# Optimization experiments

Measured on AMD Instinct MI355X. Metric: run time of the kernel, lower is better.

## Reference

```python
import jax, jax.numpy as jnp
import numpy as np
from jax import lax

H = 64  # LSTM units (hard-coded in the module)


def _lstm(x, W, U, b, return_sequences):
    """Keras-style LSTM (inference; recurrent_dropout inactive).
    x: [B, T, F]; W: [F, 4H]; U: [H, 4H]; b: [4H].
    Gate order (Keras): i, f, g(cell), o.
    """
    B = x.shape[0]
    # Precompute input contribution for all timesteps: [T, B, 4H]
    xz = jnp.einsum('btf,fg->tbg', x, W) + b

    def step(carry, z_t):
        h, c = carry
        z = z_t + h @ U  # [B, 4H]
        i = jax.nn.sigmoid(z[:, :H])
        f = jax.nn.sigmoid(z[:, H:2 * H])
        g = jnp.tanh(z[:, 2 * H:3 * H])
        o = jax.nn.sigmoid(z[:, 3 * H:])
        c = f * c + i * g
        h = o * jnp.tanh(c)
        return (h, c), h

    init = (jnp.zeros((B, H), x.dtype), jnp.zeros((B, H), x.dtype))
    (h_last, _), hs = lax.scan(step, init, xz)
    if return_sequences:
        return jnp.transpose(hs, (1, 0, 2))  # [B, T, H]
    return h_last  # [B, H]


def setup_inputs() -> dict:
    key = jax.random.key(0)
    ks = jax.random.split(key, 8)
    B, T, F = 4096, 256, 32
    s_in = 1.0 / np.sqrt(F)
    s_h = 1.0 / np.sqrt(H)
    return {
        'x': jax.random.normal(ks[0], (B, T, F), jnp.float32),
        'W1': jax.random.normal(ks[1], (F, 4 * H), jnp.float32) * s_in,
        'U1': jax.random.normal(ks[2], (H, 4 * H), jnp.float32) * s_h,
        'b1': jnp.zeros((4 * H,), jnp.float32),
        'W2': jax.random.normal(ks[3], (H, 4 * H), jnp.float32) * s_h,
        'U2': jax.random.normal(ks[4], (H, 4 * H), jnp.float32) * s_h,
        'b2': jnp.zeros((4 * H,), jnp.float32),
        'Wd': jax.random.normal(ks[5], (H, H), jnp.float32) * s_h,
        'bd': jnp.zeros((H,), jnp.float32),
        'Wo': jax.random.normal(ks[6], (H, 1), jnp.float32) * s_h,
        'bo': jnp.zeros((1,), jnp.float32),
    }


def reference(x, W1, U1, b1, W2, U2, b2, Wd, bd, Wo, bo):
    h_seq = _lstm(x, W1, U1, b1, return_sequences=True)   # hidden_lstm
    h_last = _lstm(h_seq, W2, U2, b2, return_sequences=False)  # lstm_layer
    d = jax.nn.sigmoid(h_last @ Wd + bd)  # Dense(64, sigmoid)
    return jax.nn.sigmoid(d @ Wo + bo)    # Dense(1, sigmoid) -> [B, 1]
```

## Files before the change

kernel.cpp:

```cpp
#include <hip/hip_runtime.h>


typedef __attribute__((ext_vector_type(8))) short short8;
typedef __attribute__((ext_vector_type(4))) float floatx4;
typedef __attribute__((ext_vector_type(2))) float floatx2;

__device__ __forceinline__ float ex2(float x){ return __builtin_amdgcn_exp2f(x); }
__device__ __forceinline__ float rcp_(float x){ return __builtin_amdgcn_rcpf(x); }
__device__ __forceinline__ float sigm(float x){ return rcp_(1.0f + ex2(-1.44269504f*x)); }
__device__ __forceinline__ unsigned bfbits(float f){
    unsigned u = __builtin_bit_cast(unsigned, f);
    u += 0x7FFFu + ((u >> 16) & 1u);
    return u >> 16;
}
__device__ __forceinline__ short f2bf(float f){ return (short)bfbits(f); }
__device__ __forceinline__ unsigned cvtpk(float lo, float hi){
    unsigned r;
    asm("v_cvt_pk_bf16_f32 %0, %1, %2" : "=v"(r) : "v"(lo), "v"(hi));
    return r;
}
__device__ __forceinline__ void wg_barrier_lds(){
    asm volatile("s_waitcnt lgkmcnt(0)\n\ts_barrier" ::: "memory");
}
__device__ __forceinline__ float gate_update(const floatx4& z, float& c){
    float iv = rcp_(1.0f + ex2(z[0]));
    float fv = rcp_(1.0f + ex2(z[1]));
    float rg = rcp_(1.0f + ex2(z[2]));
    float ov = rcp_(1.0f + ex2(z[3]));
    float gp = fmaf(-5.77078016f, rg, 2.88539008f);
    c = fmaf(fv, c, iv * gp);
    float th = fmaf(-2.0f, rcp_(1.0f + ex2(c)), 1.0f);
    return ov * th;
}

#define MFMA_BF16 __builtin_amdgcn_mfma_f32_16x16x32_bf16

__global__ __launch_bounds__(1024, 1)
void lstm2_tz(const float* __restrict__ x,
              const float* __restrict__ W1, const float* __restrict__ U1, const float* __restrict__ b1,
              const float* __restrict__ W2, const float* __restrict__ U2, const float* __restrict__ b2,
              const float* __restrict__ Wd, const float* __restrict__ bd,
              const float* __restrict__ Wo, const float* __restrict__ bo,
              float* __restrict__ out)
{
    __shared__ __align__(16) short h1b[2][16 * 64];
    __shared__ __align__(16) short h2b[2][16 * 64];
    __shared__ __align__(16) short xsb[2][16 * 40];
    __shared__ float psum[4][16];

    const int tid  = threadIdx.x;
    const int w    = tid >> 6;
    const bool isL1 = (w < 8);
    const int wv   = w & 7;
    const int lane = tid & 63;
    const int n    = lane & 15;
    const int q    = lane >> 4;
    const int b0   = blockIdx.x * 16;

    const float LG = 1.44269504f;

    const int ugl = n >> 2;
    const int gA  = n & 3;
    const float sA = (gA == 2) ? (2.0f * LG) : (-LG);

    const int sw   = n & 7;
    const int hro0 = n * 64 + ((q ^ sw) << 3);
    const int hro1 = n * 64 + (((4 + q) ^ sw) << 3);
    const int xro  = n * 40 + q * 8;
    const int hwo  = n * 64 + ((wv ^ sw) << 3) + q * 2;

    short8  Wa[8];
    floatx4 bC[2];
    if (isL1) {
#pragma unroll
        for (int tt = 0; tt < 2; ++tt) {
            const int un   = wv * 8 + ugl * 2 + tt;
            const int ncol = gA * 64 + un;
#pragma unroll
            for (int j = 0; j < 8; ++j) {
                const int k = q * 8 + j;
                Wa[tt * 3 + 0][j] = f2bf(W1[k * 256 + ncol] * sA);
                Wa[tt * 3 + 1][j] = f2bf(U1[k * 256 + ncol] * sA);
                Wa[tt * 3 + 2][j] = f2bf(U1[(32 + k) * 256 + ncol] * sA);
            }
#pragma unroll
            for (int r = 0; r < 4; ++r)
                bC[tt][r] = b1[r * 64 + wv * 8 + q * 2 + tt] * ((r == 2) ? (2.0f * LG) : (-LG));
        }
    } else {
#pragma unroll
        for (int tt = 0; tt < 2; ++tt) {
            const int un   = wv * 8 + ugl * 2 + tt;
            const int ncol = gA * 64 + un;
#pragma unroll
            for (int j = 0; j < 8; ++j) {
                const int k = q * 8 + j;
                Wa[tt * 4 + 0][j] = f2bf(W2[k * 256 + ncol] * sA);
                Wa[tt * 4 + 1][j] = f2bf(W2[(32 + k) * 256 + ncol] * sA);
                Wa[tt * 4 + 2][j] = f2bf(U2[k * 256 + ncol] * sA);
                Wa[tt * 4 + 3][j] = f2bf(U2[(32 + k) * 256 + ncol] * sA);
            }
#pragma unroll
            for (int r = 0; r < 4; ++r)
                bC[tt][r] = b2[r * 64 + wv * 8 + q * 2 + tt] * ((r == 2) ? (2.0f * LG) : (-LG));
        }
    }

    {
        unsigned* p1 = (unsigned*)&h1b[0][0];
        unsigned* p2 = (unsigned*)&h2b[0][0];
        for (int i = tid; i < 1024; i += 1024) { p1[i] = 0u; p2[i] = 0u; }
    }

    const int xr = tid >> 4;
    const int xc = (tid & 15) * 2;
    const float* xrow = x + (size_t)(b0 + xr) * 8192 + xc;
    floatx2 xv0;
    if (tid < 256) {
        floatx2 v = *(const floatx2*)xrow;
        *(unsigned*)&xsb[0][xr * 40 + xc] = cvtpk(v.x, v.y);
        xv0 = *(const floatx2*)(xrow + 32);
    }
    __syncthreads();

    float c[2] = {0, 0};
    floatx4 z[2];

    for (int u = 0; u <= 257; ++u) {
        const int par = u & 1, pax = par ^ 1;

        if (isL1) {
            if (u < 256) {
                const short* hR = &h1b[pax][0];
                short8 bx  = *(const short8*)&xsb[par][xro];
                short8 bh0 = *(const short8*)&hR[hro0];
                short8 bh1 = *(const short8*)&hR[hro1];
                if (tid < 256 && u < 255) {
                    *(unsigned*)&xsb[pax][xr * 40 + xc] = cvtpk(xv0.x, xv0.y);
                    if (u < 254) xv0 = *(const floatx2*)(xrow + (size_t)(u + 2) * 32);
                }
#pragma unroll
                for (int tt = 0; tt < 2; ++tt) {
                    floatx4 zz = bC[tt];
                    zz = MFMA_BF16(Wa[tt * 3 + 0], bx,  zz, 0, 0, 0);
                    zz = MFMA_BF16(Wa[tt * 3 + 1], bh0, zz, 0, 0, 0);
                    zz = MFMA_BF16(Wa[tt * 3 + 2], bh1, zz, 0, 0, 0);
                    z[tt] = zz;
                }
            }
        } else {
            if (u >= 2) {
                float hv0 = gate_update(z[0], c[0]);
                float hv1 = gate_update(z[1], c[1]);
                *(unsigned*)&h2b[par][hwo] = cvtpk(hv0, hv1);
            }
        }
        wg_barrier_lds();

        if (isL1) {
            if (u < 256) {
                float hv0 = gate_update(z[0], c[0]);
                float hv1 = gate_update(z[1], c[1]);
                *(unsigned*)&h1b[par][hwo] = cvtpk(hv0, hv1);
            }
        } else {
            if (u >= 1 && u <= 256) {
                const short* hR = &h1b[pax][0];
                const short* gR = &h2b[par][0];
                short8 bh0 = *(const short8*)&hR[hro0];
                short8 bh1 = *(const short8*)&hR[hro1];
                short8 bg0 = *(const short8*)&gR[hro0];
                short8 bg1 = *(const short8*)&gR[hro1];
#pragma unroll
                for (int tt = 0; tt < 2; ++tt) {
                    floatx4 zz = bC[tt];
                    zz = MFMA_BF16(Wa[tt * 4 + 0], bh0, zz, 0, 0, 0);
                    zz = MFMA_BF16(Wa[tt * 4 + 1], bh1, zz, 0, 0, 0);
                    zz = MFMA_BF16(Wa[tt * 4 + 2], bg0, zz, 0, 0, 0);
                    zz = MFMA_BF16(Wa[tt * 4 + 3], bg1, zz, 0, 0, 0);
                    z[tt] = zz;
                }
            }
        }
        wg_barrier_lds();
    }

    if (!isL1 && wv < 4) {
        const int colD = wv * 16 + n;
        short8 wd0, wd1;
#pragma unroll
        for (int j = 0; j < 8; ++j) {
            wd0[j] = f2bf(Wd[(q * 8 + j) * 64 + colD] * (-LG));
            wd1[j] = f2bf(Wd[(32 + q * 8 + j) * 64 + colD] * (-LG));
        }
        short8 hA0 = *(const short8*)&h2b[1][hro0];
        short8 hA1 = *(const short8*)&h2b[1][hro1];
        const float bdv = bd[colD] * (-LG);
        floatx4 dacc = { bdv, bdv, bdv, bdv };
        dacc = MFMA_BF16(hA0, wd0, dacc, 0, 0, 0);
        dacc = MFMA_BF16(hA1, wd1, dacc, 0, 0, 0);
        const float wo = Wo[colD];
#pragma unroll
        for (int r = 0; r < 4; ++r) {
            float p = rcp_(1.0f + ex2(dacc[r])) * wo;
            p += __shfl_xor(p, 1, 64);
            p += __shfl_xor(p, 2, 64);
            p += __shfl_xor(p, 4, 64);
            p += __shfl_xor(p, 8, 64);
            if (n == 0) psum[wv][q * 4 + r] = p;
        }
    }
    __syncthreads();
    if (tid < 16) {
        float s = psum[0][tid] + psum[1][tid] + psum[2][tid] + psum[3][tid] + bo[0];
        out[b0 + tid] = sigm(s);
    }
}

extern "C" void kernel_launch(void* const* d_in, const int* in_sizes, int n_in,
                              void* d_out, int out_size, void* d_ws, size_t ws_size,
                              hipStream_t stream) {
    (void)in_sizes; (void)n_in; (void)d_ws; (void)ws_size; (void)out_size;
    const float* x  = (const float*)d_in[0];
    const float* W1 = (const float*)d_in[1];
    const float* U1 = (const float*)d_in[2];
    const float* b1 = (const float*)d_in[3];
    const float* W2 = (const float*)d_in[4];
    const float* U2 = (const float*)d_in[5];
    const float* b2 = (const float*)d_in[6];
    const float* Wd = (const float*)d_in[7];
    const float* bd = (const float*)d_in[8];
    const float* Wo = (const float*)d_in[9];
    const float* bo = (const float*)d_in[10];
    lstm2_tz<<<dim3(256), dim3(1024), 0, stream>>>(
        x, W1, U1, b1, W2, U2, b2, Wd, bd, Wo, bo, (float*)d_out);
}
```

Before: 366.7 us.

## Fuse gate update into MFMA phase, halving barriers per step, share reciprocals

Restructures the two-layer wavefront-specialized time loop so each half-step does both the MFMA and the gate nonlinearity, then writes h. This leaves one workgroup barrier per timestep instead of two, and the loop is unrolled by two so buffer parities are compile-time constants. The gate function also replaces four reciprocals with one, computed on the product of the four denominators, with extra multiplies to recover each sigmoid. That shortens the critical path but risks overflow or inf when the product of the exp terms grows large.

```diff
diff --git a/kernel.cpp b/kernel.cpp
--- a/kernel.cpp
+++ b/kernel.cpp
@@ -23,10 +23,17 @@
     asm volatile("s_waitcnt lgkmcnt(0)\n\ts_barrier" ::: "memory");
 }
 __device__ __forceinline__ float gate_update(const floatx4& z, float& c){
-    float iv = rcp_(1.0f + ex2(z[0]));
-    float fv = rcp_(1.0f + ex2(z[1]));
-    float rg = rcp_(1.0f + ex2(z[2]));
-    float ov = rcp_(1.0f + ex2(z[3]));
+    float ea = 1.0f + ex2(z[0]);
+    float eb = 1.0f + ex2(z[1]);
+    float eg = 1.0f + ex2(z[2]);
+    float eo = 1.0f + ex2(z[3]);
+    float ab = ea * eb, gd = eg * eo;
+    float r  = rcp_(ab * gd);
+    float gdr = gd * r, abr = ab * r;
+    float iv = eb * gdr;
+    float fv = ea * gdr;
+    float rg = eo * abr;
+    float ov = eg * abr;
     float gp = fmaf(-5.77078016f, rg, 2.88539008f);
     c = fmaf(fv, c, iv * gp);
     float th = fmaf(-2.0f, rcp_(1.0f + ex2(c)), 1.0f);
@@ -124,66 +131,60 @@
     __syncthreads();
 
     float c[2] = {0, 0};
-    floatx4 z[2];
-
-    for (int u = 0; u <= 257; ++u) {
-        const int par = u & 1, pax = par ^ 1;
-
-        if (isL1) {
-            if (u < 256) {
-                const short* hR = &h1b[pax][0];
-                short8 bx  = *(const short8*)&xsb[par][xro];
-                short8 bh0 = *(const short8*)&hR[hro0];
-                short8 bh1 = *(const short8*)&hR[hro1];
-                if (tid < 256 && u < 255) {
-                    *(unsigned*)&xsb[pax][xr * 40 + xc] = cvtpk(xv0.x, xv0.y);
-                    if (u < 254) xv0 = *(const floatx2*)(xrow + (size_t)(u + 2) * 32);
-                }
-#pragma unroll
-                for (int tt = 0; tt < 2; ++tt) {
-                    floatx4 zz = bC[tt];
-                    zz = MFMA_BF16(Wa[tt * 3 + 0], bx,  zz, 0, 0, 0);
-                    zz = MFMA_BF16(Wa[tt * 3 + 1], bh0, zz, 0, 0, 0);
-                    zz = MFMA_BF16(Wa[tt * 3 + 2], bh1, zz, 0, 0, 0);
-                    z[tt] = zz;
-                }
-            }
-        } else {
-            if (u >= 2) {
-                float hv0 = gate_update(z[0], c[0]);
-                float hv1 = gate_update(z[1], c[1]);
-                *(unsigned*)&h2b[par][hwo] = cvtpk(hv0, hv1);
-            }
-        }
-        wg_barrier_lds();
-
-        if (isL1) {
-            if (u < 256) {
-                float hv0 = gate_update(z[0], c[0]);
-                float hv1 = gate_update(z[1], c[1]);
-                *(unsigned*)&h1b[par][hwo] = cvtpk(hv0, hv1);
-            }
-        } else {
-            if (u >= 1 && u <= 256) {
-                const short* hR = &h1b[pax][0];
-                const short* gR = &h2b[par][0];
-                short8 bh0 = *(const short8*)&hR[hro0];
-                short8 bh1 = *(const short8*)&hR[hro1];
-                short8 bg0 = *(const short8*)&gR[hro0];
-                short8 bg1 = *(const short8*)&gR[hro1];
-#pragma unroll
-                for (int tt = 0; tt < 2; ++tt) {
-                    floatx4 zz = bC[tt];
-                    zz = MFMA_BF16(Wa[tt * 4 + 0], bh0, zz, 0, 0, 0);
-                    zz = MFMA_BF16(Wa[tt * 4 + 1], bh1, zz, 0, 0, 0);
-                    zz = MFMA_BF16(Wa[tt * 4 + 2], bg0, zz, 0, 0, 0);
-                    zz = MFMA_BF16(Wa[tt * 4 + 3], bg1, zz, 0, 0, 0);
-                    z[tt] = zz;
-                }
-            }
-        }
-        wg_barrier_lds();
-    }
+
+#define LSTM_STEP(U, PAR)                                                     \
+    {                                                                         \
+        const int u_ = (U);                                                   \
+        if (isL1) {                                                           \
+            if (u_ < 256) {                                                   \
+                const short* hR = &h1b[1 - (PAR)][0];                         \
+                short8 bx  = *(const short8*)&xsb[(PAR)][xro];                \
+                short8 bh0 = *(const short8*)&hR[hro0];                       \
+                short8 bh1 = *(const short8*)&hR[hro1];                       \
+                if (tid < 256 && u_ < 255) {                                  \
+                    *(unsigned*)&xsb[1 - (PAR)][xr * 40 + xc] = cvtpk(xv0.x, xv0.y); \
+                    if (u_ < 254) xv0 = *(const floatx2*)(xrow + (size_t)(u_ + 2) * 32); \
+                }                                                             \
+                float hv[2];                                                  \
+                _Pragma("unroll")                                             \
+                for (int tt = 0; tt < 2; ++tt) {                              \
+                    floatx4 z = bC[tt];                                       \
+                    z = MFMA_BF16(Wa[tt * 3 + 0], bx,  z, 0, 0, 0);           \
+                    z = MFMA_BF16(Wa[tt * 3 + 1], bh0, z, 0, 0, 0);           \
+                    z = MFMA_BF16(Wa[tt * 3 + 2], bh1, z, 0, 0, 0);           \
+                    hv[tt] = gate_update(z, c[tt]);                           \
+                }                                                             \
+                *(unsigned*)&h1b[(PAR)][hwo] = cvtpk(hv[0], hv[1]);           \
+            }                                                                 \
+        } else {                                                              \
+            if (u_ >= 1 && u_ <= 256) {                                       \
+                const short* hR = &h1b[1 - (PAR)][0];                         \
+                const short* gR = &h2b[(PAR)][0];                             \
+                short8 bh0 = *(const short8*)&hR[hro0];                       \
+                short8 bh1 = *(const short8*)&hR[hro1];                       \
+                short8 bg0 = *(const short8*)&gR[hro0];                       \
+                short8 bg1 = *(const short8*)&gR[hro1];                       \
+                float hv[2];                                                  \
+                _Pragma("unroll")                                             \
+                for (int tt = 0; tt < 2; ++tt) {                              \
+                    floatx4 z = bC[tt];                                       \
+                    z = MFMA_BF16(Wa[tt * 4 + 0], bh0, z, 0, 0, 0);           \
+                    z = MFMA_BF16(Wa[tt * 4 + 1], bh1, z, 0, 0, 0);           \
+                    z = MFMA_BF16(Wa[tt * 4 + 2], bg0, z, 0, 0, 0);           \
+                    z = MFMA_BF16(Wa[tt * 4 + 3], bg1, z, 0, 0, 0);           \
+                    hv[tt] = gate_update(z, c[tt]);                           \
+                }                                                             \
+                *(unsigned*)&h2b[1 - (PAR)][hwo] = cvtpk(hv[0], hv[1]);       \
+            }                                                                 \
+        }                                                                     \
+        wg_barrier_lds();                                                     \
+    }
+
+    for (int uu = 0; uu < 258; uu += 2) {
+        LSTM_STEP(uu,     0)
+        LSTM_STEP(uu + 1, 1)
+    }
+#undef LSTM_STEP
 
     if (!isL1 && wv < 4) {
         const int colD = wv * 16 + n;
```

Result: faster. 330.5 us (-9.9%).
